# Kernel optimization log

Hardware: AMD Instinct MI355X
Metric: run time of the kernel (lower is better)

The kernel has to match this reference:

```python
import jax, jax.numpy as jnp
import numpy as np

N_NODES = 20
IN_DIM = 9
HID = 128
K = 5
EPS = 1e-5


def _layernorm(x, g, b):
    m = x.mean(-1, keepdims=True)
    v = ((x - m) ** 2).mean(-1, keepdims=True)
    return (x - m) / jnp.sqrt(v + EPS) * g + b


def _knn_adj(pos, k):
    # pos: [B, N, 3]; squared distances have the same ordering as torch.cdist
    d2 = jnp.sum((pos[:, :, None, :] - pos[:, None, :, :]) ** 2, axis=-1)  # [B,N,N]
    _, idx = jax.lax.top_k(-d2, k)  # k nearest (smallest distance), [B,N,k]
    # binary adjacency: row i has 1 at its k nearest columns (includes self, d=0)
    return jax.nn.one_hot(idx, pos.shape[1], dtype=pos.dtype).sum(axis=2)  # [B,N,N]


def setup_inputs() -> dict:
    key = jax.random.key(0)
    ks = jax.random.split(key, 12)
    B = 32768
    s_in = 1.0 / np.sqrt(IN_DIM)
    s_h = 1.0 / np.sqrt(HID)
    return {
        "hbond_coords": jax.random.normal(ks[0], (B, N_NODES, IN_DIM), jnp.float32),
        "w_embed": jax.random.uniform(ks[1], (IN_DIM, HID), jnp.float32, -s_in, s_in),
        "b_embed": jax.random.uniform(ks[2], (HID,), jnp.float32, -s_in, s_in),
        "w1": jax.random.uniform(ks[3], (HID, HID), jnp.float32, -s_h, s_h),
        "b1": jax.random.uniform(ks[4], (HID,), jnp.float32, -s_h, s_h),
        "w2": jax.random.uniform(ks[5], (HID, HID), jnp.float32, -s_h, s_h),
        "b2": jax.random.uniform(ks[6], (HID,), jnp.float32, -s_h, s_h),
        "g1": jnp.ones((HID,), jnp.float32),
        "be1": jnp.zeros((HID,), jnp.float32),
        "g2": jnp.ones((HID,), jnp.float32),
        "be2": jnp.zeros((HID,), jnp.float32),
    }


def reference(hbond_coords, w_embed, b_embed, w1, b1, w2, b2, g1, be1, g2, be2):
    x = hbond_coords.reshape(-1, N_NODES, IN_DIM)          # [B,20,9]
    pos = x[:, :, 6:9]                                      # [B,20,3]
    adj = _knn_adj(pos, K)                                  # [B,20,20]
    h = x @ w_embed + b_embed                               # node embed [B,20,H]
    h = jnp.einsum('bij,bjd->bid', adj, h)                  # neighbor aggregate
    h = _layernorm(h @ w1 + b1, g1, be1)
    h = jax.nn.gelu(h, approximate=False)                   # dropout is identity in eval
    h2 = jnp.einsum('bij,bjd->bid', adj, h)
    h2 = _layernorm(h2 @ w2 + b2, g2, be2)
    h = jax.nn.gelu(h + h2, approximate=False)
    return jnp.max(h, axis=1)                               # [B,H]
```

## Files before the change

### kernel.cpp

```cpp
#include <hip/hip_runtime.h>
#include <math.h>

#define N_NODES 20
#define IN_DIM  9
#define HID     128
#define K_NBR   5
#define EPS     1e-5f
#define IPB     2

#define ADJX_OFF  736
#define RES1_OFF  6160
#define SLICE     7184
#define HTSTR     24
#define HRSTR     136

typedef __attribute__((ext_vector_type(8))) short short8;
typedef __attribute__((ext_vector_type(4))) float f32x4;
typedef __attribute__((ext_vector_type(2))) float f32x2;
typedef __attribute__((ext_vector_type(2))) unsigned int u32x2;
typedef __attribute__((ext_vector_type(4))) unsigned int u32x4;

#define WB() __builtin_amdgcn_wave_barrier()

__device__ __forceinline__ unsigned short f2bf(float f) {
    unsigned u = __builtin_bit_cast(unsigned, f);
    u += 0x7fffu + ((u >> 16) & 1u);
    return (unsigned short)(u >> 16);
}
#if __has_builtin(__builtin_amdgcn_cvt_pk_bf16_f32)
typedef __attribute__((ext_vector_type(2))) __bf16 bf16x2;
__device__ __forceinline__ unsigned cvtpk(float a, float b) {
    bf16x2 r = __builtin_amdgcn_cvt_pk_bf16_f32(a, b);
    return __builtin_bit_cast(unsigned, r);
}
#else
__device__ __forceinline__ unsigned cvtpk(float a, float b) {
    return (unsigned)f2bf(a) | ((unsigned)f2bf(b) << 16);
}
#endif
__device__ __forceinline__ f32x2 unpk(unsigned u) {
    return (f32x2){ __builtin_bit_cast(float, u << 16),
                    __builtin_bit_cast(float, u & 0xffff0000u) };
}
__device__ __forceinline__ float gelu_fast(float x) {
    float x2 = x * x;
    float y  = x * fmaf(x2, 0.07135806592f, 1.5957691216f);
    float u  = __expf(fminf(y, 60.0f));
    return x * u * __builtin_amdgcn_rcpf(u + 1.0f);
}
__device__ __forceinline__ f32x2 gelu2(f32x2 x) {
    f32x2 x2 = x * x;
    f32x2 y  = x * (x2 * 0.07135806592f + 1.5957691216f);
    f32x2 u  = { __expf(fminf(y.x, 60.0f)), __expf(fminf(y.y, 60.0f)) };
    f32x2 n  = x * u;
    f32x2 d  = u + 1.0f;
    return (f32x2){ n.x * __builtin_amdgcn_rcpf(d.x), n.y * __builtin_amdgcn_rcpf(d.y) };
}
__device__ __forceinline__ f32x2 shfl2(f32x2 v, int m) {
    return (f32x2){ __shfl_xor(v.x, m), __shfl_xor(v.y, m) };
}

__device__ __forceinline__ f32x4 mfma16(short8 a, short8 b, f32x4 c) {
    return __builtin_amdgcn_mfma_f32_16x16x32_bf16(a, b, c, 0, 0, 0);
}

__global__ void prep_all(const float* __restrict__ w_embed, const float* __restrict__ b_embed,
                         const float* __restrict__ w1, const float* __restrict__ b1,
                         const float* __restrict__ w2,
                         unsigned short* __restrict__ wswM1, unsigned short* __restrict__ wsw2,
                         float* __restrict__ c1f) {
    int tid = blockIdx.x * 256 + threadIdx.x;
    if (tid < 16384) {
        int oid = tid >> 2, sub = tid & 3;
        int j = oid & 7, lane = (oid >> 3) & 63, nt = (oid >> 9) & 7;
        int k = (lane >> 4) * 8 + j;
        int n = nt * 16 + (lane & 15);
        float acc = 0.f;
        if (k < IN_DIM) {
            #pragma unroll 8
            for (int c = sub * 32; c < sub * 32 + 32; ++c)
                acc = fmaf(w_embed[k*HID + c], w1[c*HID + n], acc);
        }
        acc += __shfl_xor(acc, 1);
        acc += __shfl_xor(acc, 2);
        if (sub == 0) wswM1[oid] = (k < IN_DIM) ? f2bf(acc) : (unsigned short)0;
    } else if (tid < 16896) {
        int t2 = tid - 16384;
        int n = t2 >> 2, sub = t2 & 3;
        float cb = 0.f;
        #pragma unroll 8
        for (int c = sub * 32; c < sub * 32 + 32; ++c)
            cb = fmaf(b_embed[c], w1[c*HID + n], cb);
        cb += __shfl_xor(cb, 1);
        cb += __shfl_xor(cb, 2);
        if (sub == 0) c1f[n] = 5.0f * cb + b1[n];
    } else if (tid < 33280) {
        int i2 = tid - 16896;
        int j = i2 & 7, lane = (i2 >> 3) & 63, nt = (i2 >> 9) & 7, ks = (i2 >> 12) & 3;
        int k = ks * 32 + (lane >> 4) * 8 + j;
        int n = nt * 16 + (lane & 15);
        wsw2[i2] = f2bf(w2[k*HID + n]);
    }
}

__global__ __launch_bounds__(128, 3) void hbond_main(
    const float* __restrict__ x_in,
    const float* __restrict__ c1f, const float* __restrict__ b2,
    const float* __restrict__ g1, const float* __restrict__ be1,
    const float* __restrict__ g2, const float* __restrict__ be2,
    const unsigned short* __restrict__ wswM1, const unsigned short* __restrict__ wsw2,
    float* __restrict__ out, int nItems)
{
    __shared__ __align__(16) unsigned char smem[IPB * SLICE];

    const int l  = threadIdx.x & 63;
    const int wv = threadIdx.x >> 6;
    const int item = blockIdx.x * IPB + wv;
    if (item >= nItems) return;

    unsigned char* slice = smem + wv * SLICE;
    float*          xs   = (float*)(slice);
    unsigned short* adjx = (unsigned short*)(slice + ADJX_OFF);
    unsigned short* hrm  = (unsigned short*)(slice);
    unsigned short* tT   = (unsigned short*)(slice);
    unsigned*       resid1 = (unsigned*)(slice + RES1_OFF);

    const int ln15 = l & 15, q = l >> 4;
    const float* xb = x_in + (size_t)item * (N_NODES * IN_DIM);

    if (l == 0) *(u32x4*)(slice + HTSTR * HID * 2) = (u32x4){0,0,0,0};

    if (l < 45) ((float4*)xs)[l] = ((const float4*)xb)[l];
    WB();

    unsigned nbrp = 0;
    {
        const int rsel = (l < N_NODES) ? l : 0;
        const float px = xs[rsel*IN_DIM+6], py = xs[rsel*IN_DIM+7], pz = xs[rsel*IN_DIM+8];
        float d2[N_NODES];
        #pragma unroll
        for (int j = 0; j < N_NODES; ++j) {
            float dx = __fsub_rn(px, __shfl(px, j));
            float dy = __fsub_rn(py, __shfl(py, j));
            float dz = __fsub_rn(pz, __shfl(pz, j));
            d2[j] = __fadd_rn(__fadd_rn(__fmul_rn(dx,dx), __fmul_rn(dy,dy)), __fmul_rn(dz,dz));
        }
        unsigned used = 0u;
        #pragma unroll
        for (int k = 0; k < K_NBR; ++k) {
            float best = INFINITY; int bi = 0;
            #pragma unroll
            for (int j = 0; j < N_NODES; ++j) {
                bool take = (!((used >> j) & 1u)) && (d2[j] < best);
                best = take ? d2[j] : best;
                bi   = take ? j     : bi;
            }
            used |= (1u << bi);
            nbrp |= (unsigned)bi << (5*k);
        }
    }

    unsigned amask = 0;
    #pragma unroll
    for (int j = 0; j < K_NBR; ++j) amask |= 1u << ((nbrp >> (5*j)) & 31);
    const unsigned am0 = (unsigned)__shfl((int)amask, ln15);
    const unsigned am1 = (unsigned)__shfl((int)amask, ln15 + 16);
    short8 adjf0, adjf1;
    #pragma unroll
    for (int j = 0; j < 8; ++j) {
        adjf0[j] = (short)(((am0 >> (q*8 + j)) & 1u) ? 0x3F80 : 0);
        adjf1[j] = (short)(((am1 >> (q*8 + j)) & 1u) ? 0x3F80 : 0);
    }

    if (l < N_NODES) {
        f32x2 s01 = {0,0}, s23 = {0,0}, s45 = {0,0}, s67 = {0,0};
        float s8 = 0.f;
        #pragma unroll
        for (int j = 0; j < K_NBR; ++j) {
            const int b0 = ((nbrp >> (5*j)) & 31) * IN_DIM;
            s01 += (f32x2){xs[b0+0], xs[b0+1]};
            s23 += (f32x2){xs[b0+2], xs[b0+3]};
            s45 += (f32x2){xs[b0+4], xs[b0+5]};
            s67 += (f32x2){xs[b0+6], xs[b0+7]};
            s8  += xs[b0+8];
        }
        u32x4 p0 = { cvtpk(s01.x,s01.y), cvtpk(s23.x,s23.y), cvtpk(s45.x,s45.y), cvtpk(s67.x,s67.y) };
        u32x4 p1 = { cvtpk(s8,0.f), 0, 0, 0 };
        *(u32x4*)&adjx[l*16 + 0] = p0;
        *(u32x4*)&adjx[l*16 + 8] = p1;
    }
    WB();

    f32x4 acc[2][8];
    const int rlo = ln15, rhi = (ln15 + 16 > 19) ? 19 : ln15 + 16;

    {
        const short8 a0 = *(const short8*)&adjx[rlo*16 + (q & 1)*8];
        const short8 a1 = *(const short8*)&adjx[rhi*16 + (q & 1)*8];
        #pragma unroll
        for (int nt = 0; nt < 8; ++nt) {
            const float bv = c1f[ln15 + 16*nt];
            f32x4 c0 = (f32x4){bv, bv, bv, bv};
            const short8 bfr = *(const short8*)&wswM1[nt*512 + l*8];
            acc[0][nt] = mfma16(a0, bfr, c0);
            acc[1][nt] = mfma16(a1, bfr, c0);
        }
    }

    unsigned hU01[2][8], hU23[2][8];
    {
        float gva[8], bva[8];
        #pragma unroll
        for (int nt = 0; nt < 8; ++nt) { gva[nt] = g1[ln15+16*nt]; bva[nt] = be1[ln15+16*nt]; }
        #pragma unroll
        for (int mt = 0; mt < 2; ++mt) {
            f32x2 s01={0,0}, s23={0,0}, t01={0,0}, t23={0,0};
            #pragma unroll
            for (int nt = 0; nt < 8; ++nt) {
                f32x2 v01 = {acc[mt][nt][0], acc[mt][nt][1]};
                f32x2 v23 = {acc[mt][nt][2], acc[mt][nt][3]};
                s01 += v01; s23 += v23;
                t01 += v01*v01; t23 += v23*v23;
            }
            #pragma unroll
            for (int m = 1; m < 16; m <<= 1) {
                s01 += shfl2(s01,m); s23 += shfl2(s23,m);
                t01 += shfl2(t01,m); t23 += shfl2(t23,m);
            }
            f32x2 mean01 = s01 * (1.f/HID), mean23 = s23 * (1.f/HID);
            f32x2 var01  = t01 * (1.f/HID) - mean01*mean01;
            f32x2 var23  = t23 * (1.f/HID) - mean23*mean23;
            f32x2 rstd01 = { rsqrtf(fmaxf(var01.x,0.f)+EPS), rsqrtf(fmaxf(var01.y,0.f)+EPS) };
            f32x2 rstd23 = { rsqrtf(fmaxf(var23.x,0.f)+EPS), rsqrtf(fmaxf(var23.y,0.f)+EPS) };
            #pragma unroll
            for (int nt = 0; nt < 8; ++nt) {
                f32x2 v01 = {acc[mt][nt][0], acc[mt][nt][1]};
                f32x2 v23 = {acc[mt][nt][2], acc[mt][nt][3]};
                f32x2 h01 = gelu2((v01 - mean01) * rstd01 * gva[nt] + bva[nt]);
                f32x2 h23 = gelu2((v23 - mean23) * rstd23 * gva[nt] + bva[nt]);
                hU01[mt][nt] = cvtpk(h01.x, h01.y);
                hU23[mt][nt] = cvtpk(h23.x, h23.y);
            }
        }
    }
    WB();

    #pragma unroll
    for (int nt = 0; nt < 8; ++nt) {
        const int col = ln15 + 16*nt;
        const unsigned u01 = hU01[0][nt], u23 = hU23[0][nt];
        hrm[(q*4+0)*HRSTR + col] = (unsigned short)u01;
        hrm[(q*4+1)*HRSTR + col] = (unsigned short)(u01 >> 16);
        hrm[(q*4+2)*HRSTR + col] = (unsigned short)u23;
        hrm[(q*4+3)*HRSTR + col] = (unsigned short)(u23 >> 16);
        if (q == 0) {
            const unsigned v01 = hU01[1][nt], v23 = hU23[1][nt];
            hrm[16*HRSTR + col] = (unsigned short)v01;
            hrm[17*HRSTR + col] = (unsigned short)(v01 >> 16);
            hrm[18*HRSTR + col] = (unsigned short)v23;
            hrm[19*HRSTR + col] = (unsigned short)(v23 >> 16);
            *(u32x2*)&resid1[(nt*16 + ln15)*2] = (u32x2){v01, v23};
        }
    }
    WB();

    #pragma unroll
    for (int nt = 0; nt < 8; ++nt) { acc[0][nt] = (f32x4){0,0,0,0}; acc[1][nt] = acc[0][nt]; }
    #pragma unroll
    for (int ks = 0; ks < 4; ++ks) {
        const short8 a0 = *(const short8*)&hrm[rlo*HRSTR + ks*32 + q*8];
        const short8 a1 = *(const short8*)&hrm[rhi*HRSTR + ks*32 + q*8];
        #pragma unroll
        for (int nt = 0; nt < 8; ++nt) {
            const short8 bfr = *(const short8*)&wsw2[(ks*8 + nt)*512 + l*8];
            acc[0][nt] = mfma16(a0, bfr, acc[0][nt]);
            acc[1][nt] = mfma16(a1, bfr, acc[1][nt]);
        }
    }
    WB();

    #pragma unroll
    for (int nt = 0; nt < 8; ++nt) {
        const int col = ln15 + 16*nt;
        u32x2 w0 = { cvtpk(acc[0][nt][0], acc[0][nt][1]), cvtpk(acc[0][nt][2], acc[0][nt][3]) };
        *(u32x2*)&tT[col*HTSTR + q*4] = w0;
        if (q == 0) {
            u32x2 w1v = { cvtpk(acc[1][nt][0], acc[1][nt][1]), cvtpk(acc[1][nt][2], acc[1][nt][3]) };
            *(u32x2*)&tT[col*HTSTR + 16] = w1v;
        }
    }
    *(u32x2*)&tT[l*HTSTR + 20]        = (u32x2){0,0};
    *(u32x2*)&tT[(l + 64)*HTSTR + 20] = (u32x2){0,0};
    WB();

    #pragma unroll
    for (int nt = 0; nt < 8; ++nt) {
        const float bv = b2[ln15 + 16*nt];
        f32x4 c0 = (f32x4){bv, bv, bv, bv};
        const short8 bfr = *(const short8*)&tT[(ln15 + 16*nt)*HTSTR + q*8];
        acc[0][nt] = mfma16(adjf0, bfr, c0);
        acc[1][nt] = mfma16(adjf1, bfr, c0);
    }

    f32x2 mean01[2], mean23[2], rstd01[2], rstd23[2];
    #pragma unroll
    for (int mt = 0; mt < 2; ++mt) {
        f32x2 s01={0,0}, s23={0,0}, t01={0,0}, t23={0,0};
        #pragma unroll
        for (int nt = 0; nt < 8; ++nt) {
            f32x2 v01 = {acc[mt][nt][0], acc[mt][nt][1]};
            f32x2 v23 = {acc[mt][nt][2], acc[mt][nt][3]};
            s01 += v01; s23 += v23;
            t01 += v01*v01; t23 += v23*v23;
        }
        #pragma unroll
        for (int m = 1; m < 16; m <<= 1) {
            s01 += shfl2(s01,m); s23 += shfl2(s23,m);
            t01 += shfl2(t01,m); t23 += shfl2(t23,m);
        }
        mean01[mt] = s01 * (1.f/HID); mean23[mt] = s23 * (1.f/HID);
        f32x2 v01 = t01 * (1.f/HID) - mean01[mt]*mean01[mt];
        f32x2 v23 = t23 * (1.f/HID) - mean23[mt]*mean23[mt];
        rstd01[mt] = (f32x2){ rsqrtf(fmaxf(v01.x,0.f)+EPS), rsqrtf(fmaxf(v01.y,0.f)+EPS) };
        rstd23[mt] = (f32x2){ rsqrtf(fmaxf(v23.x,0.f)+EPS), rsqrtf(fmaxf(v23.y,0.f)+EPS) };
    }

    #pragma unroll
    for (int nt = 0; nt < 8; ++nt) {
        const int col = ln15 + 16*nt;
        const float gv = g2[col], bv = be2[col];
        f32x2 y01 = ((f32x2){acc[0][nt][0], acc[0][nt][1]} - mean01[0]) * rstd01[0] * gv + bv;
        f32x2 y23 = ((f32x2){acc[0][nt][2], acc[0][nt][3]} - mean23[0]) * rstd23[0] * gv + bv;
        f32x2 r01 = y01 + unpk(hU01[0][nt]);
        f32x2 r23 = y23 + unpk(hU23[0][nt]);
        float rmax = fmaxf(fmaxf(r01.x, r01.y), fmaxf(r23.x, r23.y));
        float rmin = fminf(fminf(r01.x, r01.y), fminf(r23.x, r23.y));
        if (q == 0) {
            f32x2 z01 = ((f32x2){acc[1][nt][0], acc[1][nt][1]} - mean01[1]) * rstd01[1] * gv + bv;
            f32x2 z23 = ((f32x2){acc[1][nt][2], acc[1][nt][3]} - mean23[1]) * rstd23[1] * gv + bv;
            const u32x2 hx = *(const u32x2*)&resid1[(nt*16 + ln15)*2];
            f32x2 w01 = z01 + unpk(hx.x);
            f32x2 w23 = z23 + unpk(hx.y);
            rmax = fmaxf(rmax, fmaxf(fmaxf(w01.x, w01.y), fmaxf(w23.x, w23.y)));
            rmin = fminf(rmin, fminf(fminf(w01.x, w01.y), fminf(w23.x, w23.y)));
        }
        rmax = fmaxf(rmax, __shfl_xor(rmax, 16)); rmin = fminf(rmin, __shfl_xor(rmin, 16));
        rmax = fmaxf(rmax, __shfl_xor(rmax, 32)); rmin = fminf(rmin, __shfl_xor(rmin, 32));
        const float m0 = fmaxf(gelu_fast(rmax), gelu_fast(rmin));
        if (l < 16) out[(size_t)item*HID + 16*nt + l] = m0;
    }
}

extern "C" void kernel_launch(void* const* d_in, const int* in_sizes, int n_in,
                              void* d_out, int out_size, void* d_ws, size_t ws_size,
                              hipStream_t stream) {
    (void)n_in; (void)out_size; (void)ws_size;
    const float* x       = (const float*)d_in[0];
    const float* w_embed = (const float*)d_in[1];
    const float* b_embed = (const float*)d_in[2];
    const float* w1      = (const float*)d_in[3];
    const float* b1      = (const float*)d_in[4];
    const float* w2      = (const float*)d_in[5];
    const float* b2      = (const float*)d_in[6];
    const float* g1      = (const float*)d_in[7];
    const float* be1     = (const float*)d_in[8];
    const float* g2      = (const float*)d_in[9];
    const float* be2     = (const float*)d_in[10];
    float* out = (float*)d_out;

    unsigned char* ws = (unsigned char*)d_ws;
    float* c1f            = (float*)(ws + 0);
    unsigned short* wswM1 = (unsigned short*)(ws + 512);
    unsigned short* wsw2  = (unsigned short*)(ws + 512 + 8192);

    const int nItems  = in_sizes[0] / (N_NODES * IN_DIM);
    const int nBlocks = (nItems + IPB - 1) / IPB;

    prep_all<<<dim3(130), dim3(256), 0, stream>>>(w_embed, b_embed, w1, b1, w2,
                                                  wswM1, wsw2, c1f);
    hbond_main<<<dim3(nBlocks), dim3(128), 0, stream>>>(
        x, c1f, b2, g1, be1, g2, be2, wswM1, wsw2, out, nItems);
}
```

Before: 294.9 us.

## Serialize row-tile MFMA phases to cut registers and raise occupancy to 4

Splits the two 16-row M-tiles (rows 0-15 and 16-19) into separate sequential passes, so only one set of 8 accumulators is live at a time instead of two. Each GEMM stage plus its LayerNorm/GELU epilogue is now done tile by tile, with an LN_STATS macro factoring out the shared statistics code. Launch bounds are raised from 3 to 4 waves per SIMD to use the freed VGPRs. In exchange, the MFMA chains are shorter and partly serialized, some B-fragment loads are repeated, and asm barriers are added to keep the compiler from merging address computations.

```diff
diff --git a/kernel.cpp b/kernel.cpp
--- a/kernel.cpp
+++ b/kernel.cpp
@@ -63,6 +63,23 @@
 __device__ __forceinline__ f32x4 mfma16(short8 a, short8 b, f32x4 c) {
     return __builtin_amdgcn_mfma_f32_16x16x32_bf16(a, b, c, 0, 0, 0);
 }
+
+#define LN_STATS(ACC, MEAN01, MEAN23, RSTD01, RSTD23)                              \
+  { f32x2 s01={0,0}, s23={0,0}, t01={0,0}, t23={0,0};                              \
+    _Pragma("unroll")                                                              \
+    for (int nt_ = 0; nt_ < 8; ++nt_) {                                            \
+      f32x2 v01_ = {ACC[nt_][0], ACC[nt_][1]};                                     \
+      f32x2 v23_ = {ACC[nt_][2], ACC[nt_][3]};                                     \
+      s01 += v01_; s23 += v23_; t01 += v01_*v01_; t23 += v23_*v23_; }              \
+    _Pragma("unroll")                                                              \
+    for (int m_ = 1; m_ < 16; m_ <<= 1) {                                          \
+      s01 += shfl2(s01,m_); s23 += shfl2(s23,m_);                                  \
+      t01 += shfl2(t01,m_); t23 += shfl2(t23,m_); }                                \
+    MEAN01 = s01 * (1.f/HID); MEAN23 = s23 * (1.f/HID);                            \
+    f32x2 va_ = t01 * (1.f/HID) - MEAN01*MEAN01;                                   \
+    f32x2 vb_ = t23 * (1.f/HID) - MEAN23*MEAN23;                                   \
+    RSTD01 = (f32x2){ rsqrtf(fmaxf(va_.x,0.f)+EPS), rsqrtf(fmaxf(va_.y,0.f)+EPS) };\
+    RSTD23 = (f32x2){ rsqrtf(fmaxf(vb_.x,0.f)+EPS), rsqrtf(fmaxf(vb_.y,0.f)+EPS) };}
 
 __global__ void prep_all(const float* __restrict__ w_embed, const float* __restrict__ b_embed,
                          const float* __restrict__ w1, const float* __restrict__ b1,
@@ -103,7 +120,7 @@
     }
 }
 
-__global__ __launch_bounds__(128, 3) void hbond_main(
+__global__ __launch_bounds__(128, 4) void hbond_main(
     const float* __restrict__ x_in,
     const float* __restrict__ c1f, const float* __restrict__ b2,
     const float* __restrict__ g1, const float* __restrict__ be1,
@@ -191,56 +208,44 @@
     }
     WB();
 
-    f32x4 acc[2][8];
+    f32x4 acc[8];
     const int rlo = ln15, rhi = (ln15 + 16 > 19) ? 19 : ln15 + 16;
 
-    {
-        const short8 a0 = *(const short8*)&adjx[rlo*16 + (q & 1)*8];
-        const short8 a1 = *(const short8*)&adjx[rhi*16 + (q & 1)*8];
+    const short8 a0g = *(const short8*)&adjx[rlo*16 + (q & 1)*8];
+    const short8 a1g = *(const short8*)&adjx[rhi*16 + (q & 1)*8];
+
+    unsigned hU01[8], hU23[8];
+
+    #pragma unroll
+    for (int nt = 0; nt < 8; ++nt) {
+        const float bv = c1f[ln15 + 16*nt];
+        acc[nt] = mfma16(a0g, *(const short8*)&wswM1[nt*512 + l*8],
+                         (f32x4){bv, bv, bv, bv});
+    }
+    {
+        f32x2 mean01, mean23, rstd01, rstd23;
+        LN_STATS(acc, mean01, mean23, rstd01, rstd23);
+        #pragma unroll
+        for (int nt = 0; nt < 8; ++nt) {
+            const int col = ln15 + 16*nt;
+            const float gv = g1[col], bv = be1[col];
+            f32x2 v01 = {acc[nt][0], acc[nt][1]};
+            f32x2 v23 = {acc[nt][2], acc[nt][3]};
+            f32x2 h01 = gelu2((v01 - mean01) * rstd01 * gv + bv);
+            f32x2 h23 = gelu2((v23 - mean23) * rstd23 * gv + bv);
+            hU01[nt] = cvtpk(h01.x, h01.y);
+            hU23[nt] = cvtpk(h23.x, h23.y);
+        }
+    }
+
+    {
+        int l8b = l * 8;
+        asm volatile("" : "+v"(l8b));
         #pragma unroll
         for (int nt = 0; nt < 8; ++nt) {
             const float bv = c1f[ln15 + 16*nt];
-            f32x4 c0 = (f32x4){bv, bv, bv, bv};
-            const short8 bfr = *(const short8*)&wswM1[nt*512 + l*8];
-            acc[0][nt] = mfma16(a0, bfr, c0);
-            acc[1][nt] = mfma16(a1, bfr, c0);
-        }
-    }
-
-    unsigned hU01[2][8], hU23[2][8];
-    {
-        float gva[8], bva[8];
-        #pragma unroll
-        for (int nt = 0; nt < 8; ++nt) { gva[nt] = g1[ln15+16*nt]; bva[nt] = be1[ln15+16*nt]; }
-        #pragma unroll
-        for (int mt = 0; mt < 2; ++mt) {
-            f32x2 s01={0,0}, s23={0,0}, t01={0,0}, t23={0,0};
-            #pragma unroll
-            for (int nt = 0; nt < 8; ++nt) {
-                f32x2 v01 = {acc[mt][nt][0], acc[mt][nt][1]};
-                f32x2 v23 = {acc[mt][nt][2], acc[mt][nt][3]};
-                s01 += v01; s23 += v23;
-                t01 += v01*v01; t23 += v23*v23;
-            }
-            #pragma unroll
-            for (int m = 1; m < 16; m <<= 1) {
-                s01 += shfl2(s01,m); s23 += shfl2(s23,m);
-                t01 += shfl2(t01,m); t23 += shfl2(t23,m);
-            }
-            f32x2 mean01 = s01 * (1.f/HID), mean23 = s23 * (1.f/HID);
-            f32x2 var01  = t01 * (1.f/HID) - mean01*mean01;
-            f32x2 var23  = t23 * (1.f/HID) - mean23*mean23;
-            f32x2 rstd01 = { rsqrtf(fmaxf(var01.x,0.f)+EPS), rsqrtf(fmaxf(var01.y,0.f)+EPS) };
-            f32x2 rstd23 = { rsqrtf(fmaxf(var23.x,0.f)+EPS), rsqrtf(fmaxf(var23.y,0.f)+EPS) };
-            #pragma unroll
-            for (int nt = 0; nt < 8; ++nt) {
-                f32x2 v01 = {acc[mt][nt][0], acc[mt][nt][1]};
-                f32x2 v23 = {acc[mt][nt][2], acc[mt][nt][3]};
-                f32x2 h01 = gelu2((v01 - mean01) * rstd01 * gva[nt] + bva[nt]);
-                f32x2 h23 = gelu2((v23 - mean23) * rstd23 * gva[nt] + bva[nt]);
-                hU01[mt][nt] = cvtpk(h01.x, h01.y);
-                hU23[mt][nt] = cvtpk(h23.x, h23.y);
-            }
+            acc[nt] = mfma16(a1g, *(const short8*)&wswM1[nt*512 + l8b],
+                             (f32x4){bv, bv, bv, bv});
         }
     }
     WB();
@@ -248,44 +253,77 @@
     #pragma unroll
     for (int nt = 0; nt < 8; ++nt) {
         const int col = ln15 + 16*nt;
-        const unsigned u01 = hU01[0][nt], u23 = hU23[0][nt];
+        const unsigned u01 = hU01[nt], u23 = hU23[nt];
         hrm[(q*4+0)*HRSTR + col] = (unsigned short)u01;
         hrm[(q*4+1)*HRSTR + col] = (unsigned short)(u01 >> 16);
         hrm[(q*4+2)*HRSTR + col] = (unsigned short)u23;
         hrm[(q*4+3)*HRSTR + col] = (unsigned short)(u23 >> 16);
-        if (q == 0) {
-            const unsigned v01 = hU01[1][nt], v23 = hU23[1][nt];
-            hrm[16*HRSTR + col] = (unsigned short)v01;
-            hrm[17*HRSTR + col] = (unsigned short)(v01 >> 16);
-            hrm[18*HRSTR + col] = (unsigned short)v23;
-            hrm[19*HRSTR + col] = (unsigned short)(v23 >> 16);
-            *(u32x2*)&resid1[(nt*16 + ln15)*2] = (u32x2){v01, v23};
-        }
-    }
-    WB();
-
-    #pragma unroll
-    for (int nt = 0; nt < 8; ++nt) { acc[0][nt] = (f32x4){0,0,0,0}; acc[1][nt] = acc[0][nt]; }
+    }
+
+    {
+        f32x2 mean01, mean23, rstd01, rstd23;
+        LN_STATS(acc, mean01, mean23, rstd01, rstd23);
+        #pragma unroll
+        for (int nt = 0; nt < 8; ++nt) {
+            const int col = ln15 + 16*nt;
+            const float gv = g1[col], bv = be1[col];
+            f32x2 v01 = {acc[nt][0], acc[nt][1]};
+            f32x2 v23 = {acc[nt][2], acc[nt][3]};
+            f32x2 h01 = gelu2((v01 - mean01) * rstd01 * gv + bv);
+            f32x2 h23 = gelu2((v23 - mean23) * rstd23 * gv + bv);
+            const unsigned v01u = cvtpk(h01.x, h01.y);
+            const unsigned v23u = cvtpk(h23.x, h23.y);
+            if (q == 0) {
+                hrm[16*HRSTR + col] = (unsigned short)v01u;
+                hrm[17*HRSTR + col] = (unsigned short)(v01u >> 16);
+                hrm[18*HRSTR + col] = (unsigned short)v23u;
+                hrm[19*HRSTR + col] = (unsigned short)(v23u >> 16);
+                *(u32x2*)&resid1[(nt*16 + ln15)*2] = (u32x2){v01u, v23u};
+            }
+        }
+    }
+    WB();
+
+    short8 a1f[4];
+    #pragma unroll
+    for (int ks = 0; ks < 4; ++ks)
+        a1f[ks] = *(const short8*)&hrm[rhi*HRSTR + ks*32 + q*8];
+
+    #pragma unroll
+    for (int nt = 0; nt < 8; ++nt) acc[nt] = (f32x4){0,0,0,0};
     #pragma unroll
     for (int ks = 0; ks < 4; ++ks) {
-        const short8 a0 = *(const short8*)&hrm[rlo*HRSTR + ks*32 + q*8];
-        const short8 a1 = *(const short8*)&hrm[rhi*HRSTR + ks*32 + q*8];
-        #pragma unroll
-        for (int nt = 0; nt < 8; ++nt) {
-            const short8 bfr = *(const short8*)&wsw2[(ks*8 + nt)*512 + l*8];
-            acc[0][nt] = mfma16(a0, bfr, acc[0][nt]);
-            acc[1][nt] = mfma16(a1, bfr, acc[1][nt]);
-        }
+        const short8 a0k = *(const short8*)&hrm[rlo*HRSTR + ks*32 + q*8];
+        #pragma unroll
+        for (int nt = 0; nt < 8; ++nt)
+            acc[nt] = mfma16(a0k, *(const short8*)&wsw2[(ks*8 + nt)*512 + l*8], acc[nt]);
     }
     WB();
 
     #pragma unroll
     for (int nt = 0; nt < 8; ++nt) {
         const int col = ln15 + 16*nt;
-        u32x2 w0 = { cvtpk(acc[0][nt][0], acc[0][nt][1]), cvtpk(acc[0][nt][2], acc[0][nt][3]) };
+        u32x2 w0 = { cvtpk(acc[nt][0], acc[nt][1]), cvtpk(acc[nt][2], acc[nt][3]) };
         *(u32x2*)&tT[col*HTSTR + q*4] = w0;
+    }
+
+    {
+        int l8c = l * 8;
+        asm volatile("" : "+v"(l8c));
+        #pragma unroll
+        for (int nt = 0; nt < 8; ++nt) acc[nt] = (f32x4){0,0,0,0};
+        #pragma unroll
+        for (int ks = 0; ks < 4; ++ks) {
+            #pragma unroll
+            for (int nt = 0; nt < 8; ++nt)
+                acc[nt] = mfma16(a1f[ks], *(const short8*)&wsw2[(ks*8 + nt)*512 + l8c], acc[nt]);
+        }
+    }
+    #pragma unroll
+    for (int nt = 0; nt < 8; ++nt) {
+        const int col = ln15 + 16*nt;
         if (q == 0) {
-            u32x2 w1v = { cvtpk(acc[1][nt][0], acc[1][nt][1]), cvtpk(acc[1][nt][2], acc[1][nt][3]) };
+            u32x2 w1v = { cvtpk(acc[nt][0], acc[nt][1]), cvtpk(acc[nt][2], acc[nt][3]) };
             *(u32x2*)&tT[col*HTSTR + 16] = w1v;
         }
     }
@@ -293,61 +331,57 @@
     *(u32x2*)&tT[(l + 64)*HTSTR + 20] = (u32x2){0,0};
     WB();
 
-    #pragma unroll
-    for (int nt = 0; nt < 8; ++nt) {
-        const float bv = b2[ln15 + 16*nt];
-        f32x4 c0 = (f32x4){bv, bv, bv, bv};
-        const short8 bfr = *(const short8*)&tT[(ln15 + 16*nt)*HTSTR + q*8];
-        acc[0][nt] = mfma16(adjf0, bfr, c0);
-        acc[1][nt] = mfma16(adjf1, bfr, c0);
-    }
-
-    f32x2 mean01[2], mean23[2], rstd01[2], rstd23[2];
-    #pragma unroll
-    for (int mt = 0; mt < 2; ++mt) {
-        f32x2 s01={0,0}, s23={0,0}, t01={0,0}, t23={0,0};
-        #pragma unroll
-        for (int nt = 0; nt < 8; ++nt) {
-            f32x2 v01 = {acc[mt][nt][0], acc[mt][nt][1]};
-            f32x2 v23 = {acc[mt][nt][2], acc[mt][nt][3]};
-            s01 += v01; s23 += v23;
-            t01 += v01*v01; t23 += v23*v23;
-        }
-        #pragma unroll
-        for (int m = 1; m < 16; m <<= 1) {
-            s01 += shfl2(s01,m); s23 += shfl2(s23,m);
-            t01 += shfl2(t01,m); t23 += shfl2(t23,m);
-        }
-        mean01[mt] = s01 * (1.f/HID); mean23[mt] = s23 * (1.f/HID);
-        f32x2 v01 = t01 * (1.f/HID) - mean01[mt]*mean01[mt];
-        f32x2 v23 = t23 * (1.f/HID) - mean23[mt]*mean23[mt];
-        rstd01[mt] = (f32x2){ rsqrtf(fmaxf(v01.x,0.f)+EPS), rsqrtf(fmaxf(v01.y,0.f)+EPS) };
-        rstd23[mt] = (f32x2){ rsqrtf(fmaxf(v23.x,0.f)+EPS), rsqrtf(fmaxf(v23.y,0.f)+EPS) };
-    }
-
-    #pragma unroll
-    for (int nt = 0; nt < 8; ++nt) {
-        const int col = ln15 + 16*nt;
-        const float gv = g2[col], bv = be2[col];
-        f32x2 y01 = ((f32x2){acc[0][nt][0], acc[0][nt][1]} - mean01[0]) * rstd01[0] * gv + bv;
-        f32x2 y23 = ((f32x2){acc[0][nt][2], acc[0][nt][3]} - mean23[0]) * rstd23[0] * gv + bv;
-        f32x2 r01 = y01 + unpk(hU01[0][nt]);
-        f32x2 r23 = y23 + unpk(hU23[0][nt]);
-        float rmax = fmaxf(fmaxf(r01.x, r01.y), fmaxf(r23.x, r23.y));
-        float rmin = fminf(fminf(r01.x, r01.y), fminf(r23.x, r23.y));
-        if (q == 0) {
-            f32x2 z01 = ((f32x2){acc[1][nt][0], acc[1][nt][1]} - mean01[1]) * rstd01[1] * gv + bv;
-            f32x2 z23 = ((f32x2){acc[1][nt][2], acc[1][nt][3]} - mean23[1]) * rstd23[1] * gv + bv;
+    float rmax1[8], rmin1[8];
+    {
+        #pragma unroll
+        for (int nt = 0; nt < 8; ++nt) {
+            const float bv = b2[ln15 + 16*nt];
+            acc[nt] = mfma16(adjf1, *(const short8*)&tT[(ln15 + 16*nt)*HTSTR + q*8],
+                             (f32x4){bv, bv, bv, bv});
+        }
+        f32x2 mean01, mean23, rstd01, rstd23;
+        LN_STATS(acc, mean01, mean23, rstd01, rstd23);
+        #pragma unroll
+        for (int nt = 0; nt < 8; ++nt) {
+            const int col = ln15 + 16*nt;
+            const float gv = g2[col], bv = be2[col];
+            f32x2 z01 = ((f32x2){acc[nt][0], acc[nt][1]} - mean01) * rstd01 * gv + bv;
+            f32x2 z23 = ((f32x2){acc[nt][2], acc[nt][3]} - mean23) * rstd23 * gv + bv;
             const u32x2 hx = *(const u32x2*)&resid1[(nt*16 + ln15)*2];
             f32x2 w01 = z01 + unpk(hx.x);
             f32x2 w23 = z23 + unpk(hx.y);
-            rmax = fmaxf(rmax, fmaxf(fmaxf(w01.x, w01.y), fmaxf(w23.x, w23.y)));
-            rmin = fminf(rmin, fminf(fminf(w01.x, w01.y), fminf(w23.x, w23.y)));
-        }
-        rmax = fmaxf(rmax, __shfl_xor(rmax, 16)); rmin = fminf(rmin, __shfl_xor(rmin, 16));
-        rmax = fmaxf(rmax, __shfl_xor(rmax, 32)); rmin = fminf(rmin, __shfl_xor(rmin, 32));
-        const float m0 = fmaxf(gelu_fast(rmax), gelu_fast(rmin));
-        if (l < 16) out[(size_t)item*HID + 16*nt + l] = m0;
+            const float mx = fmaxf(fmaxf(w01.x, w01.y), fmaxf(w23.x, w23.y));
+            const float mn = fminf(fminf(w01.x, w01.y), fminf(w23.x, w23.y));
+            rmax1[nt] = (q == 0) ? mx : -INFINITY;
+            rmin1[nt] = (q == 0) ? mn :  INFINITY;
+        }
+    }
+    {
+        int q8b = q * 8;
+        asm volatile("" : "+v"(q8b));
+        #pragma unroll
+        for (int nt = 0; nt < 8; ++nt) {
+            const float bv = b2[ln15 + 16*nt];
+            acc[nt] = mfma16(adjf0, *(const short8*)&tT[(ln15 + 16*nt)*HTSTR + q8b],
+                             (f32x4){bv, bv, bv, bv});
+        }
+        f32x2 mean01, mean23, rstd01, rstd23;
+        LN_STATS(acc, mean01, mean23, rstd01, rstd23);
+        #pragma unroll
+        for (int nt = 0; nt < 8; ++nt) {
+            const int col = ln15 + 16*nt;
+            const float gv = g2[col], bv = be2[col];
+            f32x2 y01 = ((f32x2){acc[nt][0], acc[nt][1]} - mean01) * rstd01 * gv + bv;
+            f32x2 y23 = ((f32x2){acc[nt][2], acc[nt][3]} - mean23) * rstd23 * gv + bv;
+            f32x2 r01 = y01 + unpk(hU01[nt]);
+            f32x2 r23 = y23 + unpk(hU23[nt]);
+            float rmax = fmaxf(fmaxf(fmaxf(r01.x, r01.y), fmaxf(r23.x, r23.y)), rmax1[nt]);
+            float rmin = fminf(fminf(fminf(r01.x, r01.y), fminf(r23.x, r23.y)), rmin1[nt]);
+            rmax = fmaxf(rmax, __shfl_xor(rmax, 16)); rmin = fminf(rmin, __shfl_xor(rmin, 16));
+            rmax = fmaxf(rmax, __shfl_xor(rmax, 32)); rmin = fminf(rmin, __shfl_xor(rmin, 32));
+            const float m0 = fmaxf(gelu_fast(rmax), gelu_fast(rmin));
+            if (l < 16) out[(size_t)item*HID + 16*nt + l] = m0;
+        }
     }
 }
 
```

Measured after the change: 385.7 us. 30.8% more time.
